# Kernel optimization log

Hardware: AMD Instinct MI355X
Metric: run time of the kernel (lower is better)

Reference implementation:

```python
import jax, jax.numpy as jnp
import numpy as np

BETA = 5.0
NEG = jnp.float32(-1e30)  # finite stand-in for -inf; avoids NaN on the fully-masked row 0


def setup_inputs() -> dict:
    key = jax.random.key(0)
    ks = jax.random.split(key, 6)
    B, L, d, dv, dh = 4, 4096, 512, 512, 512
    K = jax.random.normal(ks[0], (B, L, d), dtype=jnp.float32)
    V = jax.random.normal(ks[1], (B, L, dv), dtype=jnp.float32)
    # nn.Linear weights: shape (out, in), applied as x @ W.T
    Wq = jax.random.normal(ks[2], (dh, d), dtype=jnp.float32) / np.sqrt(d).astype(np.float32)
    Wk = jax.random.normal(ks[3], (dh, d), dtype=jnp.float32) / np.sqrt(d).astype(np.float32)
    Wv = jax.random.normal(ks[4], (dv, dv), dtype=jnp.float32) / np.sqrt(dv).astype(np.float32)
    Wo = jax.random.normal(ks[5], (dv, dv), dtype=jnp.float32) / np.sqrt(dv).astype(np.float32)
    return {"K": K, "V": V, "Wq": Wq, "Wk": Wk, "Wv": Wv, "Wo": Wo}


def reference(K, V, Wq, Wk, Wv, Wo):
    B, L, _ = K.shape
    dh = Wq.shape[0]
    Qh = jnp.einsum('bld,hd->blh', K, Wq)
    Kh = jnp.einsum('bld,hd->blh', K, Wk)
    Vp = jnp.einsum('bld,ed->ble', V, Wv)
    scale = jnp.float32(BETA) / jnp.sqrt(jnp.float32(dh))
    scores = jnp.einsum('bih,bjh->bij', Qh, Kh) * scale  # [B,L,L]
    # strict causal mask: attend only to j <= i-1 (triu with diagonal=0 masked)
    mask = jnp.triu(jnp.ones((L, L), dtype=bool), k=0)
    scores = jnp.where(mask[None], NEG, scores)
    attn = jax.nn.softmax(scores, axis=-1)
    # row 0 has no past: torch code zeroes it after softmax
    attn = attn.at[:, 0, :].set(0.0)
    out = jnp.einsum('bij,bjd->bid', attn, Vp)
    Vhat = jnp.einsum('bld,ed->ble', out, Wo)
    return Vhat
```

## Files before the change

kernel.cpp:

```cpp
#include <hip/hip_runtime.h>


typedef unsigned short u16;
typedef _Float16 f16;
typedef short short8 __attribute__((ext_vector_type(8)));
typedef _Float16 half8 __attribute__((ext_vector_type(8)));
typedef _Float16 half4 __attribute__((ext_vector_type(4)));
typedef float floatx4 __attribute__((ext_vector_type(4)));

#define L_SEQ 4096
#define NBATCH 4
#define DMODEL 512
#define SCALE 0.22097086912079612f
#define MMAX 30.0f

__device__ __forceinline__ u16 f2bf(float f) {
  unsigned int u = __float_as_uint(f);
  u += 0x7fffu + ((u >> 16) & 1u);
  return (u16)(u >> 16);
}
__device__ __forceinline__ float bf2f(u16 h) {
  return __uint_as_float(((unsigned int)h) << 16);
}

__device__ __forceinline__ void gl2lds16(const void* g, void* l) {
  __builtin_amdgcn_global_load_lds(
      (const __attribute__((address_space(1))) unsigned int*)g,
      (__attribute__((address_space(3))) unsigned int*)l, 16, 0, 0);
}

__global__ __launch_bounds__(256) void cvt_f16v(const float4* __restrict__ x,
                                                half4* __restrict__ o, int n4) {
  int i = blockIdx.x * 256 + threadIdx.x;
  if (i >= n4) return;
  float4 f = x[i];
  half4 h = {(f16)f.x, (f16)f.y, (f16)f.z, (f16)f.w};
  o[i] = h;
}

template <int OUT_MODE>
__global__ __launch_bounds__(256, 2) void gemm128(
    const f16* __restrict__ A, const f16* __restrict__ B,
    void* __restrict__ Cout, int ldc, long sAz, long sBz, long sCz) {
  __shared__ f16 sA[128 * 64];
  __shared__ f16 sB[128 * 64];

  const int tid = threadIdx.x;
  const int wave = tid >> 6, lane = tid & 63, quad = lane >> 4, l16 = lane & 15;
  const int wm = (wave >> 1) * 64, wn = (wave & 1) * 64;
  const int bn = blockIdx.x * 128, bm = blockIdx.y * 128, bz = blockIdx.z;

  const f16* Ab = A + (long)bz * sAz + (long)bm * 512;
  const f16* Bb = B + (long)bz * sBz + (long)bn * 512;

  floatx4 zero = {0.f, 0.f, 0.f, 0.f};
  floatx4 acc[4][4];
#pragma unroll
  for (int mi = 0; mi < 4; mi++)
#pragma unroll
    for (int ni = 0; ni < 4; ni++) acc[mi][ni] = zero;

  const int lrow = lane >> 3;
  for (int ks = 0; ks < 8; ks++) {
    __syncthreads();
#pragma unroll
    for (int i = 0; i < 4; i++) {
      int r0 = wave * 32 + i * 8;
      int r = r0 + lrow;
      int c = ((lane & 7) - r) & 7;
      gl2lds16(Ab + (long)r * 512 + ks * 64 + c * 8, &sA[r0 * 64]);
      gl2lds16(Bb + (long)r * 512 + ks * 64 + c * 8, &sB[r0 * 64]);
    }
    __syncthreads();
#pragma unroll
    for (int kk = 0; kk < 2; kk++) {
      half8 af[4], bf[4];
#pragma unroll
      for (int mi = 0; mi < 4; mi++) {
        int row = wm + mi * 16 + l16;
        int slot = (kk * 4 + quad + row) & 7;
        af[mi] = *(const half8*)&sA[row * 64 + slot * 8];
      }
#pragma unroll
      for (int ni = 0; ni < 4; ni++) {
        int row = wn + ni * 16 + l16;
        int slot = (kk * 4 + quad + row) & 7;
        bf[ni] = *(const half8*)&sB[row * 64 + slot * 8];
      }
#pragma unroll
      for (int mi = 0; mi < 4; mi++)
#pragma unroll
        for (int ni = 0; ni < 4; ni++)
          acc[mi][ni] = __builtin_amdgcn_mfma_f32_16x16x32_f16(
              af[mi], bf[ni], acc[mi][ni], 0, 0, 0);
    }
  }

#pragma unroll
  for (int mi = 0; mi < 4; mi++) {
#pragma unroll
    for (int ni = 0; ni < 4; ni++) {
#pragma unroll
      for (int rr = 0; rr < 4; rr++) {
        int row = bm + wm + mi * 16 + quad * 4 + rr;
        int col = bn + wn + ni * 16 + l16;
        long idx = (long)bz * sCz + (long)row * ldc + col;
        float v = acc[mi][ni][rr];
        if (OUT_MODE == 1) {
          ((f16*)Cout)[idx] = (f16)v;
        } else if (OUT_MODE == 3) {
          ((u16*)Cout)[idx] = f2bf(v);
        } else {
          ((float*)Cout)[idx] = v;
        }
      }
    }
  }
}

__device__ __forceinline__ int nseg_of(int qt) {
  return (qt < 12) ? ((qt + 2) >> 1) : ((qt + 4) >> 2);
}
__device__ __forceinline__ int seg_off(int qt) {
  int o = 0;
  for (int q = 2; q < qt; q++) o += 4 * nseg_of(q);
  return o;
}

#define SV_LD 40

__global__ __launch_bounds__(512, 2) void attn_kernel(
    const f16* __restrict__ Qh_g, const f16* __restrict__ Kh_g,
    const u16* __restrict__ VpT, f16* __restrict__ Ob,
    u16* __restrict__ Opart, float* __restrict__ ml) {
  __shared__ f16 sK[2][32 * 512];
  __shared__ u16 sV[2][512 * 32];
  __shared__ u16 sP[8 * 16 * SV_LD];

  const int tid = threadIdx.x;
  const int wave = tid >> 6, lane = tid & 63, quad = lane >> 4, l16 = lane & 15;

  int id = blockIdx.x;
  int qt = 31;
  for (;;) {
    int c = 4 * nseg_of(qt);
    if (id < c) break;
    id -= c;
    qt--;
  }
  const int S = nseg_of(qt);
  const int b = id / S;
  const int s = id - b * S;
  const int ktn = 4 * qt + 4;
  const int base = ktn / S, rem = ktn - base * S;
  const int len = base + (s < rem);
  const int start = s * base + (s < rem ? s : rem);

  const int q0 = qt * 128 + wave * 16;
  const long qbase = (long)b * L_SEQ + q0;

  half8 qf[16];
#pragma unroll
  for (int c = 0; c < 16; c++) {
    long a = (qbase + l16) * 512 + c * 32 + quad * 8;
    qf[c] = *(const half8*)&Qh_g[a];
  }

  floatx4 zero = {0.f, 0.f, 0.f, 0.f};
  float l_run[4] = {0.f, 0.f, 0.f, 0.f};
  floatx4 oacc[32];
#pragma unroll
  for (int nb = 0; nb < 32; nb++) oacc[nb] = zero;

  const f16* __restrict__ Kh_b = Kh_g + (long)b * L_SEQ * 512;
  const u16* __restrict__ V_b  = VpT + (long)b * (512L * L_SEQ);

  auto stage = [&](int bs, int jt) {
    const int j0 = jt * 32;
#pragma unroll
    for (int i = 0; i < 4; i++) {
      int r = wave * 4 + i;
      int k = (lane - (r & 7)) & 63;
      gl2lds16(Kh_b + (long)(j0 + r) * 512 + k * 8, &sK[bs][r * 512]);
    }
#pragma unroll
    for (int i = 0; i < 4; i++) {
      int g = wave * 4 + i;
      int d = g * 16 + (lane >> 2);
      gl2lds16(V_b + (long)d * L_SEQ + j0 + (lane & 3) * 8, &sV[bs][g * 512]);
    }
  };

  stage(0, start);

  for (int v = 0; v < len; v++) {
    const int j0 = (start + v) * 32;
    const int cur = v & 1;

    __syncthreads();
    if (v + 1 < len) stage(cur ^ 1, start + v + 1);

    const f16* kc = &sK[cur][0];
    const u16* vc = &sV[cur][0];

    floatx4 sacc0 = zero, sacc1 = zero;
    const int rot = l16 & 7;
#pragma unroll
    for (int c = 0; c < 16; c++) {
      int slot = (c * 4 + quad + rot) & 63;
      half8 b0 = *(const half8*)&kc[l16 * 512 + slot * 8];
      half8 b1 = *(const half8*)&kc[(16 + l16) * 512 + slot * 8];
      sacc0 = __builtin_amdgcn_mfma_f32_16x16x32_f16(qf[c], b0, sacc0, 0, 0, 0);
      sacc1 = __builtin_amdgcn_mfma_f32_16x16x32_f16(qf[c], b1, sacc1, 0, 0, 0);
    }

#pragma unroll
    for (int rr = 0; rr < 4; rr++) {
      int irow = q0 + quad * 4 + rr;
      float s0 = fmaf(sacc0[rr], SCALE, -MMAX);
      float s1 = fmaf(sacc1[rr], SCALE, -MMAX);
      if (j0 + l16 >= irow) s0 = -1e30f;
      if (j0 + 16 + l16 >= irow) s1 = -1e30f;
      float p0 = __expf(s0);
      float p1 = __expf(s1);
      l_run[rr] += p0 + p1;
      int pb = wave * 640 + (quad * 4 + rr) * SV_LD;
      sP[pb + l16] = f2bf(p0);
      sP[pb + 16 + l16] = f2bf(p1);
    }

    __builtin_amdgcn_s_waitcnt(0xC07F);

    short8 ap = *(const short8*)&sP[wave * 640 + l16 * SV_LD + quad * 8];
#pragma unroll
    for (int nb = 0; nb < 32; nb++) {
      short8 bv = *(const short8*)&vc[(nb * 16 + l16) * 32 + quad * 8];
      oacc[nb] = __builtin_amdgcn_mfma_f32_16x16x32_bf16(ap, bv, oacc[nb], 0, 0, 0);
    }
  }

#pragma unroll
  for (int rr = 0; rr < 4; rr++) {
    float l = l_run[rr];
    l += __shfl_xor(l, 1);
    l += __shfl_xor(l, 2);
    l += __shfl_xor(l, 4);
    l += __shfl_xor(l, 8);
    l_run[rr] = l;
  }

  if (S == 1) {
#pragma unroll
    for (int rr = 0; rr < 4; rr++) {
      int irow = q0 + quad * 4 + rr;
      float inv = (irow == 0 || l_run[rr] <= 0.f) ? 0.f : 1.0f / l_run[rr];
      long obase = ((long)b * L_SEQ + irow) * 512;
#pragma unroll
      for (int nb = 0; nb < 32; nb++) {
        Ob[obase + nb * 16 + l16] = (f16)(oacc[nb][rr] * inv);
      }
    }
  } else {
    const int slot = seg_off(qt) + b * S + s;
    const long obase = (long)slot * (128 * 512);
#pragma unroll
    for (int rr = 0; rr < 4; rr++) {
      int wrow = wave * 16 + quad * 4 + rr;
#pragma unroll
      for (int nb = 0; nb < 32; nb++) {
        Opart[obase + (long)wrow * 512 + nb * 16 + l16] = f2bf(oacc[nb][rr]);
      }
      if (l16 == 0) {
        ml[slot * 128 + wrow] = l_run[rr];
      }
    }
  }
}

__global__ __launch_bounds__(256) void attn_combine(
    const u16* __restrict__ Opart, const float* __restrict__ ml,
    f16* __restrict__ Ob) {
  const int qt = 2 + (blockIdx.x >> 2), b = blockIdx.x & 3;
  const int S = nseg_of(qt);
  const int bslot = seg_off(qt) + b * S;
  __shared__ float sInv[128];
  const int tid = threadIdx.x;
  if (tid < 128) {
    int row = tid, irow = qt * 128 + row;
    float ltot = 0.f;
    for (int s = 0; s < S; s++) ltot += ml[(bslot + s) * 128 + row];
    sInv[row] = (irow == 0 || ltot <= 0.f) ? 0.f : 1.0f / ltot;
  }
  __syncthreads();
  const int c0 = blockIdx.y * 16;
  for (int idx = tid; idx < 128 * 16; idx += 256) {
    int row = idx >> 4, cc = c0 + (idx & 15);
    float acc[8] = {0, 0, 0, 0, 0, 0, 0, 0};
    for (int s = 0; s < S; s++) {
      int4 pk = *(const int4*)&Opart[(long)(bslot + s) * 65536 + row * 512 + cc * 8];
      const u16* ph = (const u16*)&pk;
#pragma unroll
      for (int e = 0; e < 8; e++) acc[e] += bf2f(ph[e]);
    }
    float inv = sInv[row];
    f16 o[8];
#pragma unroll
    for (int e = 0; e < 8; e++) o[e] = (f16)(acc[e] * inv);
    *(int4*)&Ob[((long)b * L_SEQ + qt * 128 + row) * 512 + cc * 8] = *(int4*)o;
  }
}

extern "C" void kernel_launch(void* const* d_in, const int* in_sizes, int n_in,
                              void* d_out, int out_size, void* d_ws, size_t ws_size,
                              hipStream_t stream) {
  const float* K  = (const float*)d_in[0];
  const float* V  = (const float*)d_in[1];
  const float* Wq = (const float*)d_in[2];
  const float* Wk = (const float*)d_in[3];
  const float* Wv = (const float*)d_in[4];
  const float* Wo = (const float*)d_in[5];
  float* out = (float*)d_out;

  const int NKV = NBATCH * L_SEQ * DMODEL;
  const int NW = DMODEL * DMODEL;
  const int NSLOT = 640;

  char* w = (char*)d_ws;
  size_t off = 0;
  auto carve = [&](size_t bytes) {
    void* p = w + off;
    off += (bytes + 255) & ~(size_t)255;
    return p;
  };
  f16* Qh   = (f16*)carve((size_t)NKV * 2);
  f16* Kh   = (f16*)carve((size_t)NKV * 2);
  u16* VpTw = (u16*)carve((size_t)NKV * 2);
  f16* Obw  = (f16*)carve((size_t)NKV * 2);
  f16* Wo16 = (f16*)carve((size_t)NW * 2);
  float* mlw = (float*)carve((size_t)NSLOT * 128 * 4);
  u16* Opart = (u16*)carve((size_t)NSLOT * 65536 * 2);
  f16* K16  = (f16*)Opart;
  f16* V16  = K16 + NKV;
  f16* Wq16 = V16 + NKV;
  f16* Wk16 = Wq16 + NW;
  f16* Wv16 = Wk16 + NW;

  cvt_f16v<<<NKV / 1024, 256, 0, stream>>>((const float4*)K, (half4*)K16, NKV / 4);
  cvt_f16v<<<NKV / 1024, 256, 0, stream>>>((const float4*)V, (half4*)V16, NKV / 4);
  cvt_f16v<<<NW / 1024, 256, 0, stream>>>((const float4*)Wq, (half4*)Wq16, NW / 4);
  cvt_f16v<<<NW / 1024, 256, 0, stream>>>((const float4*)Wk, (half4*)Wk16, NW / 4);
  cvt_f16v<<<NW / 1024, 256, 0, stream>>>((const float4*)Wv, (half4*)Wv16, NW / 4);
  cvt_f16v<<<NW / 1024, 256, 0, stream>>>((const float4*)Wo, (half4*)Wo16, NW / 4);

  gemm128<1><<<dim3(4, 128, 1), 256, 0, stream>>>(
      K16, Wq16, (void*)Qh, 512, 0, 0, 0);
  gemm128<1><<<dim3(4, 128, 1), 256, 0, stream>>>(
      K16, Wk16, (void*)Kh, 512, 0, 0, 0);

  gemm128<3><<<dim3(32, 4, NBATCH), 256, 0, stream>>>(
      Wv16, V16, (void*)VpTw, L_SEQ, 0, (long)L_SEQ * 512, (long)512 * L_SEQ);

  attn_kernel<<<dim3(648, 1, 1), 512, 0, stream>>>(
      Qh, Kh, VpTw, Obw, Opart, mlw);
  attn_combine<<<dim3(120, 4, 1), 256, 0, stream>>>(Opart, mlw, Obw);

  gemm128<2><<<dim3(4, 128, 1), 256, 0, stream>>>(
      Obw, Wo16, (void*)out, 512, 0, 0, 0);

  (void)in_sizes; (void)n_in; (void)out_size; (void)ws_size;
}
```

Before: 379.2 us.

## Repartition PV matmul so each wave owns a dv slice across all query rows

The P·V stage is restructured so each wave holds four V fragments for its own 64-column slice of dv in registers and loops over all eight waves' P tiles from shared memory. Before, each wave reread the whole 512-wide V tile for only its own 16 rows. A block barrier is added so every wave's P is visible, and the V shared-memory layout gets a rotated swizzle to avoid bank conflicts. Row sums are exchanged through a new shared array so the output stores match the new ownership. The extra barrier per iteration costs some synchronisation in exchange for far fewer LDS reads of V.

```diff
diff --git a/kernel.cpp b/kernel.cpp
--- a/kernel.cpp
+++ b/kernel.cpp
@@ -136,6 +136,7 @@
   __shared__ f16 sK[2][32 * 512];
   __shared__ u16 sV[2][512 * 32];
   __shared__ u16 sP[8 * 16 * SV_LD];
+  __shared__ float sL[128];
 
   const int tid = threadIdx.x;
   const int wave = tid >> 6, lane = tid & 63, quad = lane >> 4, l16 = lane & 15;
@@ -187,7 +188,8 @@
     for (int i = 0; i < 4; i++) {
       int g = wave * 4 + i;
       int d = g * 16 + (lane >> 2);
-      gl2lds16(V_b + (long)d * L_SEQ + j0 + (lane & 3) * 8, &sV[bs][g * 512]);
+      int c = ((lane & 3) - d) & 3;
+      gl2lds16(V_b + (long)d * L_SEQ + j0 + c * 8, &sV[bs][g * 512]);
     }
   };
 
@@ -224,18 +226,29 @@
       float p0 = __expf(s0);
       float p1 = __expf(s1);
       l_run[rr] += p0 + p1;
-      int pb = wave * 640 + (quad * 4 + rr) * SV_LD;
+      int pb = wave * (16 * SV_LD) + (quad * 4 + rr) * SV_LD;
       sP[pb + l16] = f2bf(p0);
       sP[pb + 16 + l16] = f2bf(p1);
     }
 
+    __builtin_amdgcn_sched_barrier(0);
     __builtin_amdgcn_s_waitcnt(0xC07F);
-
-    short8 ap = *(const short8*)&sP[wave * 640 + l16 * SV_LD + quad * 8];
-#pragma unroll
-    for (int nb = 0; nb < 32; nb++) {
-      short8 bv = *(const short8*)&vc[(nb * 16 + l16) * 32 + quad * 8];
-      oacc[nb] = __builtin_amdgcn_mfma_f32_16x16x32_bf16(ap, bv, oacc[nb], 0, 0, 0);
+    __builtin_amdgcn_s_barrier();
+    __builtin_amdgcn_sched_barrier(0);
+
+    short8 vf[4];
+#pragma unroll
+    for (int nbl = 0; nbl < 4; nbl++) {
+      int dvr = wave * 64 + nbl * 16 + l16;
+      vf[nbl] = *(const short8*)&vc[dvr * 32 + ((quad + l16) & 3) * 8];
+    }
+#pragma unroll
+    for (int qg = 0; qg < 8; qg++) {
+      short8 ap = *(const short8*)&sP[qg * (16 * SV_LD) + l16 * SV_LD + quad * 8];
+#pragma unroll
+      for (int nbl = 0; nbl < 4; nbl++)
+        oacc[qg * 4 + nbl] =
+            __builtin_amdgcn_mfma_f32_16x16x32_bf16(ap, vf[nbl], oacc[qg * 4 + nbl], 0, 0, 0);
     }
   }
 
@@ -248,31 +261,45 @@
     l += __shfl_xor(l, 8);
     l_run[rr] = l;
   }
+  if (l16 == 0) {
+#pragma unroll
+    for (int rr = 0; rr < 4; rr++) sL[wave * 16 + quad * 4 + rr] = l_run[rr];
+  }
+  __syncthreads();
 
   if (S == 1) {
 #pragma unroll
-    for (int rr = 0; rr < 4; rr++) {
-      int irow = q0 + quad * 4 + rr;
-      float inv = (irow == 0 || l_run[rr] <= 0.f) ? 0.f : 1.0f / l_run[rr];
-      long obase = ((long)b * L_SEQ + irow) * 512;
-#pragma unroll
-      for (int nb = 0; nb < 32; nb++) {
-        Ob[obase + nb * 16 + l16] = (f16)(oacc[nb][rr] * inv);
+    for (int qg = 0; qg < 8; qg++) {
+#pragma unroll
+      for (int rr = 0; rr < 4; rr++) {
+        int row = qg * 16 + quad * 4 + rr;
+        int irow = qt * 128 + row;
+        float lv = sL[row];
+        float inv = (irow == 0 || lv <= 0.f) ? 0.f : 1.0f / lv;
+        long obase = ((long)b * L_SEQ + irow) * 512 + wave * 64;
+#pragma unroll
+        for (int nbl = 0; nbl < 4; nbl++)
+          Ob[obase + nbl * 16 + l16] = (f16)(oacc[qg * 4 + nbl][rr] * inv);
       }
     }
   } else {
     const int slot = seg_off(qt) + b * S + s;
-    const long obase = (long)slot * (128 * 512);
-#pragma unroll
-    for (int rr = 0; rr < 4; rr++) {
-      int wrow = wave * 16 + quad * 4 + rr;
-#pragma unroll
-      for (int nb = 0; nb < 32; nb++) {
-        Opart[obase + (long)wrow * 512 + nb * 16 + l16] = f2bf(oacc[nb][rr]);
-      }
-      if (l16 == 0) {
-        ml[slot * 128 + wrow] = l_run[rr];
-      }
+    const long obase0 = (long)slot * (128 * 512);
+#pragma unroll
+    for (int qg = 0; qg < 8; qg++) {
+#pragma unroll
+      for (int rr = 0; rr < 4; rr++) {
+        int row = qg * 16 + quad * 4 + rr;
+        long ob = obase0 + (long)row * 512 + wave * 64;
+#pragma unroll
+        for (int nbl = 0; nbl < 4; nbl++)
+          Opart[ob + nbl * 16 + l16] = f2bf(oacc[qg * 4 + nbl][rr]);
+      }
+    }
+    if (l16 == 0) {
+#pragma unroll
+      for (int rr = 0; rr < 4; rr++)
+        ml[slot * 128 + wave * 16 + quad * 4 + rr] = l_run[rr];
     }
   }
 }
```

New measurement: 358.2 us. 5.5% less time.
